# Optimization experiments

Hardware: AMD Instinct MI355X
Metric: run time of the kernel (lower is better)

## Reference

```python
import jax, jax.numpy as jnp
import numpy as np
import math

WP, WF = 10, 10      # past/future window
EPS = 1e-8           # torch cosine_similarity eps
CLIP = 1.0 - 1e-6    # keep arccos (and its grad) finite
MAXN = 110           # hard-coded alpha width in the module


def setup_inputs() -> dict:
    key = jax.random.key(0)
    k1, k2, k3, k4, k5, k6 = jax.random.split(key, 6)
    B, L, G, N, D = 32, 110, 512, 40, 300
    node_features = jax.random.normal(k1, (B, L, G), jnp.float32)
    knowledge = jax.random.normal(k2, (B, L, N, D), jnp.float32)
    anew = jax.random.uniform(k3, (B, L, N), jnp.float32)
    var_sem = 2.0 / (G + G)
    var_con = 2.0 / (D + D)
    weight_sem = jax.random.normal(k4, (G, G), jnp.float32) * var_sem
    weight_con = jax.random.normal(k5, (D, D), jnp.float32) * var_con
    text_len = jax.random.randint(k6, (B,), 55, L + 1, jnp.int32)
    return dict(node_features=node_features, knowledge=knowledge, anew=anew,
                weight_sem=weight_sem, weight_con=weight_con, text_len=text_len)


def reference(node_features, knowledge, anew, weight_sem, weight_con, text_len):
    B, L, G = node_features.shape
    N = knowledge.shape[2]
    dt = node_features.dtype

    # window + validity mask, replaces per-(i,j) python slicing: [B, j, k]
    j = jnp.arange(L)[:, None]
    k = jnp.arange(L)[None, :]
    cur = text_len[:, None, None]
    mask = (k >= j - WP) & (k <= j + WF)
    mask = mask[None] & (k[None, :, :] <= cur - 1) & (j[None, :, :] < cur)
    fmask = mask.astype(dt)

    # ---- semantic branch: score = 1 - acos(cos_sim(f_j, W_sem f_k))/pi, windowed softmax
    att_sem = jnp.einsum('st,blt->bls', weight_sem, node_features)      # [B,L,G]
    num = jnp.einsum('bjg,bkg->bjk', node_features, att_sem)
    nf = jnp.maximum(jnp.linalg.norm(node_features, axis=-1), EPS)      # [B,L]
    na = jnp.maximum(jnp.linalg.norm(att_sem, axis=-1), EPS)            # [B,L]
    cos = num / (nf[:, :, None] * na[:, None, :])
    score = 1.0 - jnp.arccos(jnp.clip(cos, -CLIP, CLIP)) / math.pi
    neg = jnp.finfo(dt).min
    s = jnp.where(mask, score, neg)
    s = s - jnp.max(s, axis=-1, keepdims=True)
    e = jnp.exp(s) * fmask
    alphas_sem = e / jnp.maximum(jnp.sum(e, axis=-1, keepdims=True), EPS)  # [B,L,L]

    # ---- affinity transform of anew: v -> (||[v, v/2] - [0.5, 0]|| - 0.06467)/0.607468
    anew_aff = (jnp.sqrt((anew - 0.5) ** 2 + (0.5 * anew) ** 2) - 0.06467) / 0.607468

    # ---- contextual branch: windowed sum_n |cos_sim(aff_feat_{k,n}, knowledge_{j,n})|
    att_con = jnp.einsum('blns,st->blnt', knowledge, weight_con)        # [B,L,N,D]
    aff_feat = att_con * anew_aff[..., None]                            # [B,L,N,D]
    num_c = jnp.einsum('bknd,bjnd->bjkn', aff_feat, knowledge)          # [B,j,k,N]
    n_f = jnp.maximum(jnp.linalg.norm(aff_feat, axis=-1), EPS)          # [B,k,N]
    n_k = jnp.maximum(jnp.linalg.norm(knowledge, axis=-1), EPS)         # [B,j,N]
    cos_c = num_c / (n_f[:, None, :, :] * n_k[:, :, None, :])
    alphas_con = 10.0 * jnp.sum(jnp.abs(cos_c), axis=-1) * fmask        # [B,j,k]

    out = 0.5 * alphas_sem + 0.5 * alphas_con                           # [B,L,L]
    if L < MAXN:  # module hard-codes width 110
        out = jnp.pad(out, ((0, 0), (0, 0), (0, MAXN - L)))
    return out
```

## Files before the change

kernel.cpp:

```cpp
#include <hip/hip_runtime.h>
#include <hip/hip_bf16.h>
#include <math.h>

constexpr int Bb   = 32;
constexpr int Ls   = 110;
constexpr int Gs   = 512;
constexpr int Ns   = 40;
constexpr int Ds   = 300;
constexpr int WPc  = 10;
constexpr int WFc  = 10;
constexpr int MAXNc = 110;
constexpr float EPSf  = 1e-8f;
constexpr float CLIPf = 1.0f - 1e-6f;
constexpr int BL = Bb * Ls;
constexpr int Mrows = BL * Ns;
constexpr int KST = 320;
constexpr int RG2 = Mrows / 128;

typedef __attribute__((ext_vector_type(8))) short short8_t;
typedef __attribute__((ext_vector_type(4))) short short4_t;
typedef __attribute__((ext_vector_type(4))) float floatx4;

__device__ __forceinline__ unsigned short bf16r(float f) {
  unsigned u = __float_as_uint(f);
  u += 0x7fffu + ((u >> 16) & 1u);
  return (unsigned short)(u >> 16);
}

__device__ __forceinline__ unsigned pkbf(float lo, float hi) {
  unsigned a = __float_as_uint(lo), b = __float_as_uint(hi);
  a += 0x7fffu + ((a >> 16) & 1u);
  b += 0x7fffu + ((b >> 16) & 1u);
  return (a >> 16) | (b & 0xffff0000u);
}

__device__ __forceinline__ short8_t cvt8(const float4 v0, const float4 v1) {
  union { short8_t s; unsigned u[4]; } p;
  p.u[0] = pkbf(v0.x, v0.y);
  p.u[1] = pkbf(v0.z, v0.w);
  p.u[2] = pkbf(v1.x, v1.y);
  p.u[3] = pkbf(v1.z, v1.w);
  return p.s;
}

__global__ __launch_bounds__(256) void transpose_wsem(const float* __restrict__ w,
                                                      float* __restrict__ wt) {
  __shared__ float tile[32][33];
  const int bx = blockIdx.x * 32;
  const int by = blockIdx.y * 32;
  const int tx = threadIdx.x;
  const int ty = threadIdx.y;
#pragma unroll
  for (int r = ty; r < 32; r += 8)
    tile[r][tx] = w[(by + r) * Gs + (bx + tx)];
  __syncthreads();
#pragma unroll
  for (int r = ty; r < 32; r += 8)
    wt[(bx + r) * Gs + (by + tx)] = tile[tx][r];
}

__global__ __launch_bounds__(64) void wctf_prep(const float* __restrict__ wc,
                                                short* __restrict__ wctf) {
  const int fid = blockIdx.x;
  const int nb = fid / 10, c = fid % 10;
  const int lane = threadIdx.x;
  const int t = nb * 16 + (lane & 15);
  const int s0 = c * 32 + (lane >> 4) * 8;
  short8_t v;
#pragma unroll
  for (int e = 0; e < 8; ++e) {
    const int s = s0 + e;
    const float f = (s < Ds && t < Ds) ? wc[s * Ds + t] : 0.f;
    v[e] = (short)bf16r(f);
  }
  *reinterpret_cast<short8_t*>(wctf + ((size_t)fid * 64 + lane) * 8) = v;
}

__global__ __launch_bounds__(512) void sem_gemm(const float* __restrict__ nf,
                                                const float* __restrict__ wt,
                                                float* __restrict__ att_sem,
                                                float* __restrict__ na_arr) {
  const int bl0 = blockIdx.x * 8;
  const int s = threadIdx.x;
  const float* __restrict__ x0 = nf + (size_t)bl0 * Gs;
  float acc[8];
#pragma unroll
  for (int r = 0; r < 8; ++r) acc[r] = 0.f;
#pragma unroll 4
  for (int t = 0; t < Gs; ++t) {
    const float wv = wt[t * Gs + s];
#pragma unroll
    for (int r = 0; r < 8; ++r) acc[r] = fmaf(wv, x0[r * Gs + t], acc[r]);
  }
#pragma unroll
  for (int r = 0; r < 8; ++r) att_sem[(size_t)(bl0 + r) * Gs + s] = acc[r];

  __shared__ float partial[8][8];
  const int wave = s >> 6, lane = s & 63;
#pragma unroll
  for (int r = 0; r < 8; ++r) {
    float v = acc[r] * acc[r];
#pragma unroll
    for (int off = 32; off > 0; off >>= 1) v += __shfl_xor(v, off);
    if (lane == 0) partial[r][wave] = v;
  }
  __syncthreads();
  if (s < 8) {
    float sum = 0.f;
#pragma unroll
    for (int w2 = 0; w2 < 8; ++w2) sum += partial[s][w2];
    na_arr[bl0 + s] = fmaxf(sqrtf(sum), EPSf);
  }
}

__global__ __launch_bounds__(256) void sem_attn(const float* __restrict__ nf,
                                                const float* __restrict__ att_sem,
                                                const float* __restrict__ na_arr,
                                                const int* __restrict__ tlen,
                                                float* __restrict__ out) {
  const int blk = blockIdx.x;
  const int b = blk / Ls, j = blk % Ls;
  const int len = tlen[b];
  float* __restrict__ orow = out + (size_t)(b * Ls + j) * MAXNc;
  if (j >= len) {
    for (int k = threadIdx.x; k < MAXNc; k += 256) orow[k] = 0.f;
    return;
  }
  const int k0 = max(j - WPc, 0);
  const int k1 = min(j + WFc, len - 1);
  const int nk = k1 - k0 + 1;

  __shared__ float xs[Gs];
  __shared__ float sc[21];
  __shared__ float red[4];

  const float* __restrict__ x = nf + (size_t)(b * Ls + j) * Gs;
  float ss = 0.f;
  for (int t = threadIdx.x; t < Gs; t += 256) {
    const float v = x[t];
    xs[t] = v;
    ss += v * v;
  }
  const int wave = threadIdx.x >> 6, lane = threadIdx.x & 63;
#pragma unroll
  for (int off = 32; off > 0; off >>= 1) ss += __shfl_xor(ss, off);
  if (lane == 0) red[wave] = ss;
  __syncthreads();
  const float nfn = fmaxf(sqrtf(red[0] + red[1] + red[2] + red[3]), EPSf);

  for (int i = wave; i < nk; i += 4) {
    const int k = k0 + i;
    const float* __restrict__ as = att_sem + (size_t)(b * Ls + k) * Gs;
    float d = 0.f;
#pragma unroll
    for (int t = lane; t < Gs; t += 64) d = fmaf(xs[t], as[t], d);
#pragma unroll
    for (int off = 32; off > 0; off >>= 1) d += __shfl_xor(d, off);
    if (lane == 0) {
      float cs = d / (nfn * na_arr[b * Ls + k]);
      cs = fminf(fmaxf(cs, -CLIPf), CLIPf);
      sc[i] = 1.0f - acosf(cs) * (float)(1.0 / M_PI);
    }
  }
  __syncthreads();
  if (threadIdx.x == 0) {
    float m = -1e30f;
    for (int i = 0; i < nk; ++i) m = fmaxf(m, sc[i]);
    red[0] = m;
  }
  __syncthreads();
  const float m = red[0];
  if ((int)threadIdx.x < nk) sc[threadIdx.x] = expf(sc[threadIdx.x] - m);
  __syncthreads();
  if (threadIdx.x == 0) {
    float s = 0.f;
    for (int i = 0; i < nk; ++i) s += sc[i];
    red[1] = 1.0f / fmaxf(s, EPSf);
  }
  __syncthreads();
  const float inv = red[1];
  for (int k = threadIdx.x; k < MAXNc; k += 256) {
    float v = 0.f;
    if (k >= k0 && k <= k1) v = 0.5f * sc[k - k0] * inv;
    orow[k] = v;
  }
}

__global__ __launch_bounds__(256, 4) void con_gemm_mfma(const float* __restrict__ kn,
                                                        const short* __restrict__ wctf,
                                                        const int* __restrict__ tlen,
                                                        unsigned short* __restrict__ ybar,
                                                        float* __restrict__ rowss) {
  const int lin = blockIdx.x;
  const int xcd = lin & 7, slot = lin >> 3;
  const int m = slot & 3;
  const int g = xcd + 8 * (slot >> 2);
  if (g >= RG2) return;

  const int tid = threadIdx.x;
  const int wave = tid >> 6, lane = tid & 63;
  const int quad = lane >> 4, l16 = lane & 15;
  const int wrow = g * 128 + wave * 32;

  {
    bool any = false;
    for (int bl = wrow / Ns; bl <= (wrow + 31) / Ns; ++bl)
      any |= (bl % Ls) < tlen[bl / Ls];
    if (!any) return;
  }

  const int nb0 = m * 5;
  const short* __restrict__ bbase = wctf + (size_t)nb0 * 5120;

  const float* arow[2];
#pragma unroll
  for (int tt = 0; tt < 2; ++tt)
    arow[tt] = kn + (size_t)(wrow + tt * 16 + l16) * Ds + quad * 8;

  floatx4 acc[2][5];
#pragma unroll
  for (int tt = 0; tt < 2; ++tt)
#pragma unroll
    for (int i = 0; i < 5; ++i) acc[tt][i] = (floatx4){0.f, 0.f, 0.f, 0.f};

  float4 F0[2], F1[2];
#pragma unroll
  for (int tt = 0; tt < 2; ++tt) {
    F0[tt] = *reinterpret_cast<const float4*>(arow[tt]);
    F1[tt] = *reinterpret_cast<const float4*>(arow[tt] + 4);
  }

#pragma unroll
  for (int c = 0; c < 10; ++c) {
    short8_t bfr[5];
#pragma unroll
    for (int i = 0; i < 5; ++i)
      bfr[i] = *reinterpret_cast<const short8_t*>(
          bbase + ((size_t)(i * 10 + c) * 64 + lane) * 8);
    short8_t Af[2];
#pragma unroll
    for (int tt = 0; tt < 2; ++tt) Af[tt] = cvt8(F0[tt], F1[tt]);
    if (c < 8) {
#pragma unroll
      for (int tt = 0; tt < 2; ++tt) {
        F0[tt] = *reinterpret_cast<const float4*>(arow[tt] + (c + 1) * 32);
        F1[tt] = *reinterpret_cast<const float4*>(arow[tt] + (c + 1) * 32 + 4);
      }
    } else if (c == 8) {
#pragma unroll
      for (int tt = 0; tt < 2; ++tt) {
        float4 v0 = make_float4(0.f, 0.f, 0.f, 0.f);
        float4 v1 = make_float4(0.f, 0.f, 0.f, 0.f);
        if (quad == 0) {
          v0 = *reinterpret_cast<const float4*>(arow[tt] + 288);
          v1 = *reinterpret_cast<const float4*>(arow[tt] + 292);
        } else if (quad == 1) {
          v0 = *reinterpret_cast<const float4*>(arow[tt] + 288);
        }
        F0[tt] = v0;
        F1[tt] = v1;
      }
    }
#pragma unroll
    for (int i = 0; i < 5; ++i)
#pragma unroll
      for (int tt = 0; tt < 2; ++tt)
        acc[tt][i] = __builtin_amdgcn_mfma_f32_16x16x32_bf16(Af[tt], bfr[i],
                                                             acc[tt][i], 0, 0, 0);
  }

  const int n0 = m * 80;
#pragma unroll
  for (int tt = 0; tt < 2; ++tt) {
    const int row0 = wrow + tt * 16;
    const int blA = row0 / Ns, blB = (row0 + 15) / Ns;
    const bool alive = ((blA % Ls) < tlen[blA / Ls]) | ((blB % Ls) < tlen[blB / Ls]);
    if (!alive) continue;

#pragma unroll
    for (int r = 0; r < 4; ++r) {
      float p = 0.f;
#pragma unroll
      for (int i = 0; i < 5; ++i) p = fmaf(acc[tt][i][r], acc[tt][i][r], p);
      p += __shfl_xor(p, 1);
      p += __shfl_xor(p, 2);
      p += __shfl_xor(p, 4);
      p += __shfl_xor(p, 8);
      if (l16 == 0) atomicAdd(&rowss[row0 + quad * 4 + r], p);
    }
#pragma unroll
    for (int i = 0; i < 5; ++i) {
      const int col = n0 + i * 16 + l16;
#pragma unroll
      for (int r = 0; r < 4; ++r)
        ybar[(size_t)(row0 + quad * 4 + r) * KST + col] = bf16r(acc[tt][i][r]);
    }
  }
}

__global__ __launch_bounds__(512) void con_attn_mfma(const float* __restrict__ kn,
                                                     const unsigned short* __restrict__ ybar,
                                                     const float* __restrict__ rowss,
                                                     const float* __restrict__ anew,
                                                     const int* __restrict__ tlen,
                                                     float* __restrict__ out) {
  const int lin = blockIdx.x;
  const int xcd = lin & 7, slot = lin >> 3;
  const int b = xcd * 4 + slot / 7;
  const int jt = slot % 7;
  const int j0 = jt * 16;
  const int len = tlen[b];
  if (j0 >= len) return;
  const int kbase = min(max(j0 - WPc, 0), Ls - 48);

  const int tid = threadIdx.x;
  const int wave = tid >> 6, lane = tid & 63;
  const int quad = lane >> 4, l16 = lane & 15;

  __shared__ float red[8][768];

  const int jj = min(j0 + l16, Ls - 1);
  const size_t blj = (size_t)(b * Ls + jj);

  float outacc[3][4];
#pragma unroll
  for (int t = 0; t < 3; ++t)
#pragma unroll
    for (int r = 0; r < 4; ++r) outacc[t][r] = 0.f;

  const unsigned short* yrow[3];
  int krow_m[3];
#pragma unroll
  for (int t = 0; t < 3; ++t) {
    const int k = kbase + t * 16 + l16;
    yrow[t] = ybar + (size_t)(b * Ls + k) * Ns * KST;
    krow_m[t] = (b * Ls + k) * Ns;
  }

  for (int ni = 0; ni < 5; ++ni) {
    const int n = wave + ni * 8;
    const float* __restrict__ arow = kn + (blj * Ns + n) * (size_t)Ds + quad * 8;

    float w_t[3];
#pragma unroll
    for (int t = 0; t < 3; ++t) {
      const int mm = krow_m[t] + n;
      const float a = anew[mm];
      const float ssqk = rowss[mm];
      const float aff = (sqrtf((a - 0.5f) * (a - 0.5f) + 0.25f * a * a) - 0.06467f) *
                        (1.0f / 0.607468f);
      w_t[t] = aff / fmaxf(aff * sqrtf(ssqk), EPSf);
    }

    floatx4 S[3];
#pragma unroll
    for (int t = 0; t < 3; ++t) S[t] = (floatx4){0.f, 0.f, 0.f, 0.f};
    float ssq = 0.f;

#pragma unroll
    for (int c = 0; c < 10; ++c) {
      float4 v0 = make_float4(0.f, 0.f, 0.f, 0.f);
      float4 v1 = make_float4(0.f, 0.f, 0.f, 0.f);
      if (c < 9) {
        v0 = *reinterpret_cast<const float4*>(arow + c * 32);
        v1 = *reinterpret_cast<const float4*>(arow + c * 32 + 4);
      } else {
        if (quad == 0) {
          v0 = *reinterpret_cast<const float4*>(arow + 288);
          v1 = *reinterpret_cast<const float4*>(arow + 292);
        } else if (quad == 1) {
          v0 = *reinterpret_cast<const float4*>(arow + 288);
        }
      }
      ssq += v0.x * v0.x + v0.y * v0.y + v0.z * v0.z + v0.w * v0.w +
             v1.x * v1.x + v1.y * v1.y + v1.z * v1.z + v1.w * v1.w;
      const short8_t afrag = cvt8(v0, v1);
#pragma unroll
      for (int t = 0; t < 3; ++t) {
        const short8_t bfrag = *reinterpret_cast<const short8_t*>(
            yrow[t] + (size_t)n * KST + c * 32 + quad * 8);
        S[t] = __builtin_amdgcn_mfma_f32_16x16x32_bf16(afrag, bfrag, S[t], 0, 0, 0);
      }
    }

    ssq += __shfl_xor(ssq, 16);
    ssq += __shfl_xor(ssq, 32);
    const float kinv = 1.0f / fmaxf(sqrtf(ssq), EPSf);

#pragma unroll
    for (int r = 0; r < 4; ++r) {
      const float kv = __shfl(kinv, quad * 4 + r);
#pragma unroll
      for (int t = 0; t < 3; ++t)
        outacc[t][r] = fmaf(kv * w_t[t], fabsf(S[t][r]), outacc[t][r]);
    }
  }

#pragma unroll
  for (int t = 0; t < 3; ++t)
#pragma unroll
    for (int r = 0; r < 4; ++r)
      red[wave][(quad * 4 + r) * 48 + t * 16 + l16] = outacc[t][r];
  __syncthreads();

  for (int idx = tid; idx < 768; idx += 512) {
    float s = 0.f;
#pragma unroll
    for (int w = 0; w < 8; ++w) s += red[w][idx];
    const int j = j0 + idx / 48;
    const int k = kbase + idx % 48;
    if (j < len && k < len && k >= j - WPc && k <= j + WFc)
      out[(size_t)(b * Ls + j) * MAXNc + k] += 5.0f * s;
  }
}

extern "C" void kernel_launch(void* const* d_in, const int* in_sizes, int n_in,
                              void* d_out, int out_size, void* d_ws, size_t ws_size,
                              hipStream_t stream) {
  const float* nf   = (const float*)d_in[0];
  const float* kn   = (const float*)d_in[1];
  const float* anew = (const float*)d_in[2];
  const float* wsem = (const float*)d_in[3];
  const float* wcon = (const float*)d_in[4];
  const int*   tlen = (const int*)d_in[5];
  float* out = (float*)d_out;

  float* att_sem = (float*)d_ws;
  float* na_arr  = att_sem + (size_t)BL * Gs;
  float* wt      = na_arr + BL;
  short* wctf    = (short*)(wt + (size_t)Gs * Gs);
  float* rowss   = (float*)(wctf + 200 * 64 * 8);
  unsigned short* ybar = (unsigned short*)(rowss + Mrows);

  hipMemsetAsync(rowss, 0, (size_t)Mrows * sizeof(float), stream);
  transpose_wsem<<<dim3(16, 16), dim3(32, 8), 0, stream>>>(wsem, wt);
  wctf_prep<<<200, 64, 0, stream>>>(wcon, wctf);
  sem_gemm<<<BL / 8, 512, 0, stream>>>(nf, wt, att_sem, na_arr);
  sem_attn<<<BL, 256, 0, stream>>>(nf, att_sem, na_arr, tlen, out);
  con_gemm_mfma<<<4416, 256, 0, stream>>>(kn, wctf, tlen, ybar, rowss);
  con_attn_mfma<<<Bb * 7, 512, 0, stream>>>(kn, ybar, rowss, anew, tlen, out);
}
```

Before: 516.7 us.

## Fuse contextual GEMM and attention into one LDS-pipelined kernel

Replaces the separate knowledge×W_con GEMM kernel, which wrote a bf16 intermediate and per-row sum-of-squares to global memory, with a single kernel. Each block handles one batch and a 16-wide k tile. For each of the 40 n slices it stages knowledge rows into double-buffered LDS, runs the projection with W_con fragments held in registers, and consumes the result in the attention MFMA one iteration later. This removes the large global intermediate, the memset and the global atomics. The costs are only 224 blocks of 640 threads with three waves doing the attention phase, one barrier per n, and heavy register use for the resident weight fragments.

```diff
diff --git a/kernel.cpp b/kernel.cpp
--- a/kernel.cpp
+++ b/kernel.cpp
@@ -13,12 +13,9 @@
 constexpr float EPSf  = 1e-8f;
 constexpr float CLIPf = 1.0f - 1e-6f;
 constexpr int BL = Bb * Ls;
-constexpr int Mrows = BL * Ns;
-constexpr int KST = 320;
-constexpr int RG2 = Mrows / 128;
+constexpr int BPITCH = 328;
 
 typedef __attribute__((ext_vector_type(8))) short short8_t;
-typedef __attribute__((ext_vector_type(4))) short short4_t;
 typedef __attribute__((ext_vector_type(4))) float floatx4;
 
 __device__ __forceinline__ unsigned short bf16r(float f) {
@@ -186,231 +183,144 @@
   }
 }
 
-__global__ __launch_bounds__(256, 4) void con_gemm_mfma(const float* __restrict__ kn,
-                                                        const short* __restrict__ wctf,
-                                                        const int* __restrict__ tlen,
-                                                        unsigned short* __restrict__ ybar,
-                                                        float* __restrict__ rowss) {
+__global__ __launch_bounds__(640, 3) void con_fused(const float* __restrict__ kn,
+                                                    const short* __restrict__ wctf,
+                                                    const float* __restrict__ anew,
+                                                    const int* __restrict__ tlen,
+                                                    float* __restrict__ out) {
   const int lin = blockIdx.x;
   const int xcd = lin & 7, slot = lin >> 3;
-  const int m = slot & 3;
-  const int g = xcd + 8 * (slot >> 2);
-  if (g >= RG2) return;
+  const int b = xcd * 4 + slot / 7;
+  const int kt = slot % 7;
+  const int k0 = kt * 16;
+  const int len = tlen[b];
+  if (k0 >= len) return;
+  const int jbase = min(max(k0 - WPc, 0), Ls - 48);
 
   const int tid = threadIdx.x;
   const int wave = tid >> 6, lane = tid & 63;
   const int quad = lane >> 4, l16 = lane & 15;
-  const int wrow = g * 128 + wave * 32;
-
-  {
-    bool any = false;
-    for (int bl = wrow / Ns; bl <= (wrow + 31) / Ns; ++bl)
-      any |= (bl % Ls) < tlen[bl / Ls];
-    if (!any) return;
-  }
-
-  const int nb0 = m * 5;
-  const short* __restrict__ bbase = wctf + (size_t)nb0 * 5120;
-
-  const float* arow[2];
+
+  __shared__ short klds[2][16 * BPITCH];
+  __shared__ short ylds[2][16 * BPITCH];
+  __shared__ float rowss[40][16];
+
+  reinterpret_cast<float*>(rowss)[tid] = 0.f;
+
+  short8_t Awc[2][10];
 #pragma unroll
   for (int tt = 0; tt < 2; ++tt)
-    arow[tt] = kn + (size_t)(wrow + tt * 16 + l16) * Ds + quad * 8;
-
-  floatx4 acc[2][5];
-#pragma unroll
-  for (int tt = 0; tt < 2; ++tt)
-#pragma unroll
-    for (int i = 0; i < 5; ++i) acc[tt][i] = (floatx4){0.f, 0.f, 0.f, 0.f};
-
-  float4 F0[2], F1[2];
-#pragma unroll
-  for (int tt = 0; tt < 2; ++tt) {
-    F0[tt] = *reinterpret_cast<const float4*>(arow[tt]);
-    F1[tt] = *reinterpret_cast<const float4*>(arow[tt] + 4);
-  }
-
-#pragma unroll
-  for (int c = 0; c < 10; ++c) {
-    short8_t bfr[5];
-#pragma unroll
-    for (int i = 0; i < 5; ++i)
-      bfr[i] = *reinterpret_cast<const short8_t*>(
-          bbase + ((size_t)(i * 10 + c) * 64 + lane) * 8);
-    short8_t Af[2];
-#pragma unroll
-    for (int tt = 0; tt < 2; ++tt) Af[tt] = cvt8(F0[tt], F1[tt]);
-    if (c < 8) {
-#pragma unroll
-      for (int tt = 0; tt < 2; ++tt) {
-        F0[tt] = *reinterpret_cast<const float4*>(arow[tt] + (c + 1) * 32);
-        F1[tt] = *reinterpret_cast<const float4*>(arow[tt] + (c + 1) * 32 + 4);
-      }
-    } else if (c == 8) {
-#pragma unroll
-      for (int tt = 0; tt < 2; ++tt) {
-        float4 v0 = make_float4(0.f, 0.f, 0.f, 0.f);
-        float4 v1 = make_float4(0.f, 0.f, 0.f, 0.f);
-        if (quad == 0) {
-          v0 = *reinterpret_cast<const float4*>(arow[tt] + 288);
-          v1 = *reinterpret_cast<const float4*>(arow[tt] + 292);
-        } else if (quad == 1) {
-          v0 = *reinterpret_cast<const float4*>(arow[tt] + 288);
-        }
-        F0[tt] = v0;
-        F1[tt] = v1;
-      }
-    }
-#pragma unroll
-    for (int i = 0; i < 5; ++i)
-#pragma unroll
-      for (int tt = 0; tt < 2; ++tt)
-        acc[tt][i] = __builtin_amdgcn_mfma_f32_16x16x32_bf16(Af[tt], bfr[i],
-                                                             acc[tt][i], 0, 0, 0);
-  }
-
-  const int n0 = m * 80;
-#pragma unroll
-  for (int tt = 0; tt < 2; ++tt) {
-    const int row0 = wrow + tt * 16;
-    const int blA = row0 / Ns, blB = (row0 + 15) / Ns;
-    const bool alive = ((blA % Ls) < tlen[blA / Ls]) | ((blB % Ls) < tlen[blB / Ls]);
-    if (!alive) continue;
-
-#pragma unroll
-    for (int r = 0; r < 4; ++r) {
-      float p = 0.f;
-#pragma unroll
-      for (int i = 0; i < 5; ++i) p = fmaf(acc[tt][i][r], acc[tt][i][r], p);
-      p += __shfl_xor(p, 1);
-      p += __shfl_xor(p, 2);
-      p += __shfl_xor(p, 4);
-      p += __shfl_xor(p, 8);
-      if (l16 == 0) atomicAdd(&rowss[row0 + quad * 4 + r], p);
-    }
-#pragma unroll
-    for (int i = 0; i < 5; ++i) {
-      const int col = n0 + i * 16 + l16;
-#pragma unroll
-      for (int r = 0; r < 4; ++r)
-        ybar[(size_t)(row0 + quad * 4 + r) * KST + col] = bf16r(acc[tt][i][r]);
-    }
-  }
-}
-
-__global__ __launch_bounds__(512) void con_attn_mfma(const float* __restrict__ kn,
-                                                     const unsigned short* __restrict__ ybar,
-                                                     const float* __restrict__ rowss,
-                                                     const float* __restrict__ anew,
-                                                     const int* __restrict__ tlen,
-                                                     float* __restrict__ out) {
-  const int lin = blockIdx.x;
-  const int xcd = lin & 7, slot = lin >> 3;
-  const int b = xcd * 4 + slot / 7;
-  const int jt = slot % 7;
-  const int j0 = jt * 16;
-  const int len = tlen[b];
-  if (j0 >= len) return;
-  const int kbase = min(max(j0 - WPc, 0), Ls - 48);
-
-  const int tid = threadIdx.x;
-  const int wave = tid >> 6, lane = tid & 63;
-  const int quad = lane >> 4, l16 = lane & 15;
-
-  __shared__ float red[8][768];
-
-  const int jj = min(j0 + l16, Ls - 1);
-  const size_t blj = (size_t)(b * Ls + jj);
-
-  float outacc[3][4];
-#pragma unroll
-  for (int t = 0; t < 3; ++t)
-#pragma unroll
-    for (int r = 0; r < 4; ++r) outacc[t][r] = 0.f;
-
-  const unsigned short* yrow[3];
-  int krow_m[3];
-#pragma unroll
-  for (int t = 0; t < 3; ++t) {
-    const int k = kbase + t * 16 + l16;
-    yrow[t] = ybar + (size_t)(b * Ls + k) * Ns * KST;
-    krow_m[t] = (b * Ls + k) * Ns;
-  }
-
-  for (int ni = 0; ni < 5; ++ni) {
-    const int n = wave + ni * 8;
-    const float* __restrict__ arow = kn + (blj * Ns + n) * (size_t)Ds + quad * 8;
-
-    float w_t[3];
-#pragma unroll
-    for (int t = 0; t < 3; ++t) {
-      const int mm = krow_m[t] + n;
-      const float a = anew[mm];
-      const float ssqk = rowss[mm];
-      const float aff = (sqrtf((a - 0.5f) * (a - 0.5f) + 0.25f * a * a) - 0.06467f) *
-                        (1.0f / 0.607468f);
-      w_t[t] = aff / fmaxf(aff * sqrtf(ssqk), EPSf);
-    }
-
-    floatx4 S[3];
-#pragma unroll
-    for (int t = 0; t < 3; ++t) S[t] = (floatx4){0.f, 0.f, 0.f, 0.f};
+#pragma unroll
+    for (int c = 0; c < 10; ++c)
+      Awc[tt][c] = *reinterpret_cast<const short8_t*>(
+          wctf + ((size_t)((wave + 10 * tt) * 10 + c) * 64 + lane) * 8);
+
+  const int srow = tid / 40, scol = tid % 40;
+  const float* __restrict__ ksrc =
+      kn + ((size_t)(b * Ls + min(k0 + srow, Ls - 1)) * Ns) * Ds + scol * 8;
+
+  auto STAGE = [&](int np) {
+    float4 v0 = make_float4(0.f, 0.f, 0.f, 0.f);
+    float4 v1 = make_float4(0.f, 0.f, 0.f, 0.f);
+    const float* src = ksrc + (size_t)np * Ds;
+    if (scol < 37) {
+      v0 = *reinterpret_cast<const float4*>(src);
+      v1 = *reinterpret_cast<const float4*>(src + 4);
+    } else if (scol == 37) {
+      v0 = *reinterpret_cast<const float4*>(src);
+    }
+    *reinterpret_cast<short8_t*>(&klds[np & 1][srow * BPITCH + scol * 8]) =
+        cvt8(v0, v1);
+  };
+
+  float outacc[4] = {0.f, 0.f, 0.f, 0.f};
+  const int jrow = jbase + wave * 16 + l16;
+  const float* __restrict__ ajbase =
+      kn + ((size_t)(b * Ls + jrow) * Ns) * Ds + quad * 8;
+  const int mmk = (b * Ls + min(k0 + l16, Ls - 1)) * Ns;
+
+  auto PHASE3 = [&](int n) {
+    const int buf = n & 1;
+    const float* aj = ajbase + (size_t)n * Ds;
+    floatx4 S = (floatx4){0.f, 0.f, 0.f, 0.f};
     float ssq = 0.f;
-
 #pragma unroll
     for (int c = 0; c < 10; ++c) {
       float4 v0 = make_float4(0.f, 0.f, 0.f, 0.f);
       float4 v1 = make_float4(0.f, 0.f, 0.f, 0.f);
       if (c < 9) {
-        v0 = *reinterpret_cast<const float4*>(arow + c * 32);
-        v1 = *reinterpret_cast<const float4*>(arow + c * 32 + 4);
+        v0 = *reinterpret_cast<const float4*>(aj + c * 32);
+        v1 = *reinterpret_cast<const float4*>(aj + c * 32 + 4);
       } else {
         if (quad == 0) {
-          v0 = *reinterpret_cast<const float4*>(arow + 288);
-          v1 = *reinterpret_cast<const float4*>(arow + 292);
+          v0 = *reinterpret_cast<const float4*>(aj + 288);
+          v1 = *reinterpret_cast<const float4*>(aj + 292);
         } else if (quad == 1) {
-          v0 = *reinterpret_cast<const float4*>(arow + 288);
+          v0 = *reinterpret_cast<const float4*>(aj + 288);
         }
       }
       ssq += v0.x * v0.x + v0.y * v0.y + v0.z * v0.z + v0.w * v0.w +
              v1.x * v1.x + v1.y * v1.y + v1.z * v1.z + v1.w * v1.w;
       const short8_t afrag = cvt8(v0, v1);
-#pragma unroll
-      for (int t = 0; t < 3; ++t) {
-        const short8_t bfrag = *reinterpret_cast<const short8_t*>(
-            yrow[t] + (size_t)n * KST + c * 32 + quad * 8);
-        S[t] = __builtin_amdgcn_mfma_f32_16x16x32_bf16(afrag, bfrag, S[t], 0, 0, 0);
-      }
-    }
-
+      const short8_t bfrag = *reinterpret_cast<const short8_t*>(
+          &ylds[buf][l16 * BPITCH + c * 32 + quad * 8]);
+      S = __builtin_amdgcn_mfma_f32_16x16x32_bf16(afrag, bfrag, S, 0, 0, 0);
+    }
     ssq += __shfl_xor(ssq, 16);
     ssq += __shfl_xor(ssq, 32);
     const float kinv = 1.0f / fmaxf(sqrtf(ssq), EPSf);
-
+    const float a = anew[mmk + n];
+    const float aff = (sqrtf((a - 0.5f) * (a - 0.5f) + 0.25f * a * a) - 0.06467f) *
+                      (1.0f / 0.607468f);
+    const float w = aff / fmaxf(aff * sqrtf(rowss[n][l16]), EPSf);
 #pragma unroll
     for (int r = 0; r < 4; ++r) {
       const float kv = __shfl(kinv, quad * 4 + r);
-#pragma unroll
-      for (int t = 0; t < 3; ++t)
-        outacc[t][r] = fmaf(kv * w_t[t], fabsf(S[t][r]), outacc[t][r]);
-    }
-  }
-
-#pragma unroll
-  for (int t = 0; t < 3; ++t)
-#pragma unroll
-    for (int r = 0; r < 4; ++r)
-      red[wave][(quad * 4 + r) * 48 + t * 16 + l16] = outacc[t][r];
-  __syncthreads();
-
-  for (int idx = tid; idx < 768; idx += 512) {
-    float s = 0.f;
-#pragma unroll
-    for (int w = 0; w < 8; ++w) s += red[w][idx];
-    const int j = j0 + idx / 48;
-    const int k = kbase + idx % 48;
-    if (j < len && k < len && k >= j - WPc && k <= j + WFc)
-      out[(size_t)(b * Ls + j) * MAXNc + k] += 5.0f * s;
+      outacc[r] = fmaf(kv * w, fabsf(S[r]), outacc[r]);
+    }
+  };
+
+  STAGE(0);
+  __syncthreads();
+
+  for (int n = 0; n < 40; ++n) {
+    if (n < 39) STAGE(n + 1);
+    {
+      const int buf = n & 1;
+      floatx4 a0 = (floatx4){0.f, 0.f, 0.f, 0.f};
+      floatx4 a1 = (floatx4){0.f, 0.f, 0.f, 0.f};
+#pragma unroll
+      for (int c = 0; c < 10; ++c) {
+        const short8_t bfrag = *reinterpret_cast<const short8_t*>(
+            &klds[buf][l16 * BPITCH + c * 32 + quad * 8]);
+        a0 = __builtin_amdgcn_mfma_f32_16x16x32_bf16(Awc[0][c], bfrag, a0, 0, 0, 0);
+        a1 = __builtin_amdgcn_mfma_f32_16x16x32_bf16(Awc[1][c], bfrag, a1, 0, 0, 0);
+      }
+      float ss = 0.f;
+#pragma unroll
+      for (int r = 0; r < 4; ++r) {
+        ss += a0[r] * a0[r] + a1[r] * a1[r];
+        ylds[buf][l16 * BPITCH + wave * 16 + quad * 4 + r] = (short)bf16r(a0[r]);
+        ylds[buf][l16 * BPITCH + (wave + 10) * 16 + quad * 4 + r] =
+            (short)bf16r(a1[r]);
+      }
+      ss += __shfl_xor(ss, 16);
+      ss += __shfl_xor(ss, 32);
+      if (quad == 0) atomicAdd(&rowss[n][l16], ss);
+    }
+    if (wave < 3 && n >= 1) PHASE3(n - 1);
+    __syncthreads();
+  }
+
+  if (wave < 3) {
+    PHASE3(39);
+#pragma unroll
+    for (int r = 0; r < 4; ++r) {
+      const int j = jbase + wave * 16 + quad * 4 + r;
+      const int k = k0 + l16;
+      if (j < len && k < len && k >= j - WPc && k <= j + WFc)
+        out[(size_t)(b * Ls + j) * MAXNc + k] += 5.0f * outacc[r];
+    }
   }
 }
 
@@ -429,14 +339,10 @@
   float* na_arr  = att_sem + (size_t)BL * Gs;
   float* wt      = na_arr + BL;
   short* wctf    = (short*)(wt + (size_t)Gs * Gs);
-  float* rowss   = (float*)(wctf + 200 * 64 * 8);
-  unsigned short* ybar = (unsigned short*)(rowss + Mrows);
-
-  hipMemsetAsync(rowss, 0, (size_t)Mrows * sizeof(float), stream);
+
   transpose_wsem<<<dim3(16, 16), dim3(32, 8), 0, stream>>>(wsem, wt);
   wctf_prep<<<200, 64, 0, stream>>>(wcon, wctf);
   sem_gemm<<<BL / 8, 512, 0, stream>>>(nf, wt, att_sem, na_arr);
   sem_attn<<<BL, 256, 0, stream>>>(nf, att_sem, na_arr, tlen, out);
-  con_gemm_mfma<<<4416, 256, 0, stream>>>(kn, wctf, tlen, ybar, rowss);
-  con_attn_mfma<<<Bb * 7, 512, 0, stream>>>(kn, ybar, rowss, anew, tlen, out);
-}
+  con_fused<<<224, 640, 0, stream>>>(kn, wctf, anew, tlen, out);
+}
```

Result: slower. 641.5 us (+24.1%).
